# Kernel optimization log

Measured on AMD Instinct MI355X. Metric: run time of the kernel, lower is better.

Reference implementation:

```python
import jax, jax.numpy as jnp
import numpy as np

N = 100000   # n_nodes
E = 600000   # n_edges
D = 128      # cfg_node_encoding_dim
L = 4        # nr_layers
EPS = 1e-5


def setup_inputs() -> dict:
    key = jax.random.key(0)
    k0, k1, k2, k3 = jax.random.split(key, 4)
    x = jax.random.normal(k0, (N, D), dtype=jnp.float32)
    edge_index = jax.random.randint(k1, (2, E), 0, N, dtype=jnp.int32)
    W = jax.random.normal(k2, (L, D, D), dtype=jnp.float32) * (1.0 / np.sqrt(D))
    b = jax.random.normal(k3, (L, D), dtype=jnp.float32) * 0.01
    gamma = jnp.ones((L, D), dtype=jnp.float32)
    beta = jnp.zeros((L, D), dtype=jnp.float32)
    return {"x": x, "W": W, "b": b, "gamma": gamma, "beta": beta,
            "edge_index": edge_index}


def _gcn_layer(x, W, b, src_sl, dst_sl, norm):
    # PyG GCNConv: h = x @ W, then symmetric-normalized aggregation + bias
    h = x @ W                                  # [N, D]
    msg = h[src_sl] * norm[:, None]            # [E+N, D] gather + scale
    out = jax.ops.segment_sum(msg, dst_sl, num_segments=N)  # scatter-add
    return out + b


def _layer_norm(x, gamma, beta):
    mu = jnp.mean(x, axis=-1, keepdims=True)
    var = jnp.mean(jnp.square(x - mu), axis=-1, keepdims=True)
    return (x - mu) * jax.lax.rsqrt(var + EPS) * gamma + beta


def reference(x, W, b, gamma, beta, edge_index):
    src, dst = edge_index[0], edge_index[1]
    loops = jnp.arange(N, dtype=edge_index.dtype)
    src_sl = jnp.concatenate([src, loops])     # add_self_loops=True
    dst_sl = jnp.concatenate([dst, loops])
    deg = jax.ops.segment_sum(jnp.ones(E + N, dtype=x.dtype), dst_sl,
                              num_segments=N)
    dinv = jnp.where(deg > 0, jax.lax.rsqrt(deg), 0.0)
    norm = dinv[src_sl] * dinv[dst_sl]         # D^{-1/2} (A+I) D^{-1/2}
    h = x
    for i in range(L):
        h = _gcn_layer(h, W[i], b[i], src_sl, dst_sl, norm)
        h = jax.nn.relu(h)
        # dropout is identity in eval mode
        h = _layer_norm(h, gamma[i], beta[i])
    return h
```

## Files before the change

kernel.cpp:

```cpp
#include <hip/hip_runtime.h>
#include <hip/hip_bf16.h>

#define D_DIM 128
#define AST 136
#define CST 132

typedef __attribute__((ext_vector_type(8))) short short8v;
typedef __attribute__((ext_vector_type(4))) short short4v;
typedef __attribute__((ext_vector_type(4))) float floatx4;

__device__ __forceinline__ short f2bf(float x) {
    unsigned u = __builtin_bit_cast(unsigned, x);
    unsigned r = u + 0x7fff + ((u >> 16) & 1);
    return (short)(r >> 16);
}
__device__ __forceinline__ float bflo(unsigned p) {
    return __builtin_bit_cast(float, p << 16);
}
__device__ __forceinline__ float bfhi(unsigned p) {
    return __builtin_bit_cast(float, p & 0xffff0000u);
}


__global__ __launch_bounds__(256) void init_kernel(int* __restrict__ deg,
                                                   int* __restrict__ packedi,
                                                   int* __restrict__ ovcnt, int n16) {
    int i = blockIdx.x * blockDim.x + threadIdx.x;
    if (i < n16) {
        packedi[i] = i >> 4;
        if ((i & 15) == 0) deg[i >> 4] = 0;
    }
    if (i == 0) *ovcnt = 0;
}

__global__ void fill2_kernel(const int* __restrict__ src, const int* __restrict__ dst,
                             int* __restrict__ deg, int* __restrict__ packedi,
                             int2* __restrict__ ov, int* __restrict__ ovcnt, int e) {
    int i = blockIdx.x * blockDim.x + threadIdx.x;
    if (i >= e) return;
    int s = src[i], d = dst[i];
    int j = atomicAdd(&deg[d], 1);
    if (j < 16) {
        packedi[(size_t)d * 16 + j] = s;
    } else {
        int k = atomicAdd(ovcnt, 1);
        ov[k] = make_int2(d, s);
    }
}

__global__ void dinv_kernel(const int* __restrict__ deg, float* __restrict__ dinv, int n) {
    int i = blockIdx.x * blockDim.x + threadIdx.x;
    if (i < n) dinv[i] = rsqrtf((float)deg[i] + 1.0f);
}

__global__ __launch_bounds__(256) void wt_prep_kernel(const float* __restrict__ W,
                                                      short* __restrict__ Wt, int total) {
    int o = blockIdx.x * blockDim.x + threadIdx.x;
    if (o >= total) return;
    int l = o >> 14;
    int r = o & 16383;
    int nn = r >> 7;
    int k  = r & 127;
    Wt[o] = f2bf(W[(size_t)l * 16384 + (size_t)k * 128 + nn]);
}

template <bool IN_F32>
__global__ __launch_bounds__(256) void gemm_mfma_kernel(const void* __restrict__ Xv,
                                                        const short* __restrict__ Wt,
                                                        short* __restrict__ H, int n) {
    __shared__ short Alds[64 * AST];
    const int t    = threadIdx.x;
    const int wv   = t >> 6;
    const int lane = t & 63;
    const int m    = lane & 15;
    const int quad = lane >> 4;
    const int row0 = blockIdx.x * 64;

    short8v bfr[2][4];
    #pragma unroll
    for (int c = 0; c < 2; ++c) {
        const short* bp = Wt + (size_t)((wv * 2 + c) * 16 + m) * D_DIM + quad * 8;
        #pragma unroll
        for (int kt = 0; kt < 4; ++kt)
            bfr[c][kt] = *(const short8v*)(bp + kt * 32);
    }

    if constexpr (IN_F32) {
        const float* X = (const float*)Xv;
        #pragma unroll
        for (int i = 0; i < 8; ++i) {
            int q  = t + i * 256;
            int r  = q >> 5;
            int k4 = q & 31;
            int row = row0 + r;
            float4 v = make_float4(0.f, 0.f, 0.f, 0.f);
            if (row < n) v = *(const float4*)(X + (size_t)row * D_DIM + k4 * 4);
            short4v s;
            s.x = f2bf(v.x); s.y = f2bf(v.y); s.z = f2bf(v.z); s.w = f2bf(v.w);
            *(short4v*)(&Alds[r * AST + k4 * 4]) = s;
        }
    } else {
        const short* X = (const short*)Xv;
        #pragma unroll
        for (int i = 0; i < 4; ++i) {
            int q  = t + i * 256;
            int r  = q >> 4;
            int kc = q & 15;
            int row = row0 + r;
            short8v v = {0,0,0,0,0,0,0,0};
            if (row < n) v = *(const short8v*)(X + (size_t)row * D_DIM + kc * 8);
            *(short8v*)(&Alds[r * AST + kc * 8]) = v;
        }
    }
    __syncthreads();

    floatx4 acc[4][2];
    #pragma unroll
    for (int rt = 0; rt < 4; ++rt) {
        const short* ab = &Alds[(rt * 16 + m) * AST + quad * 8];
        short8v afr[4];
        #pragma unroll
        for (int kt = 0; kt < 4; ++kt) afr[kt] = *(const short8v*)(ab + kt * 32);

        #pragma unroll
        for (int c = 0; c < 2; ++c) {
            floatx4 a = (floatx4){0.f, 0.f, 0.f, 0.f};
            #pragma unroll
            for (int kt = 0; kt < 4; ++kt)
                a = __builtin_amdgcn_mfma_f32_16x16x32_bf16(afr[kt], bfr[c][kt], a, 0, 0, 0);
            acc[rt][c] = a;
        }
    }
    __syncthreads();

    #pragma unroll
    for (int rt = 0; rt < 4; ++rt) {
        #pragma unroll
        for (int c = 0; c < 2; ++c) {
            const int col = (wv * 2 + c) * 16 + m;
            #pragma unroll
            for (int r = 0; r < 4; ++r)
                Alds[(rt * 16 + quad * 4 + r) * CST + col] = f2bf(acc[rt][c][r]);
        }
    }
    __syncthreads();

    #pragma unroll
    for (int i = 0; i < 4; ++i) {
        int q  = t + i * 256;
        int r  = q >> 4;
        int kc = q & 15;
        int row = row0 + r;
        if (row < n)
            *(short8v*)(H + (size_t)row * D_DIM + kc * 8) = *(const short8v*)(&Alds[r * CST + kc * 8]);
    }
}

template <bool OUT_BF16>
__global__ __launch_bounds__(256) void agg_kernel(const short* __restrict__ Hb,
                                                  const int* __restrict__ packedi,
                                                  const int* __restrict__ deg,
                                                  const float* __restrict__ dinv,
                                                  const int2* __restrict__ ov,
                                                  const int* __restrict__ ovcnt,
                                                  const float* __restrict__ bias,
                                                  const float* __restrict__ gamma,
                                                  const float* __restrict__ beta,
                                                  void* __restrict__ Yv, int n) {
    const int wave = __builtin_amdgcn_readfirstlane(threadIdx.x >> 6);
    const int lane = threadIdx.x & 63;
    const int vA = (blockIdx.x * 4 + wave) * 2;
    if (vA >= n) return;
    const bool hasB = (vA + 1) < n;
    const int vB = hasB ? vA + 1 : vA;

    const int cntA = deg[vA];
    const int cntB = hasB ? deg[vB] : 0;
    const float dvA = dinv[vA];
    const float dvB = dinv[vB];

    const int sl = lane & 31;
    const int pk = packedi[(size_t)vA * 16 + (hasB ? sl : (sl & 15))];
    const float2 bb = ((const float2*)bias)[lane];
    const float2 gg = ((const float2*)gamma)[lane];
    const float2 be = ((const float2*)beta)[lane];
    const unsigned psA = ((const unsigned*)(Hb + (size_t)vA * D_DIM))[lane];
    const unsigned psB = ((const unsigned*)(Hb + (size_t)vB * D_DIM))[lane];

    float axA = bflo(psA) * dvA;
    float ayA = bfhi(psA) * dvA;
    float axB = bflo(psB) * dvB;
    float ayB = bfhi(psB) * dvB;

    unsigned p[16];
    float    w[16];
    #pragma unroll
    for (int j = 0; j < 8; ++j) {
        const int sA = __builtin_amdgcn_readlane(pk, j);
        const int sB = __builtin_amdgcn_readlane(pk, 16 + j);
        p[j]     = ((const unsigned*)(Hb + (size_t)sA * D_DIM))[lane];
        p[8 + j] = ((const unsigned*)(Hb + (size_t)sB * D_DIM))[lane];
        w[j]     = (j < cntA) ? dinv[sA] : 0.f;
        w[8 + j] = (j < cntB) ? dinv[sB] : 0.f;
    }
    #pragma unroll
    for (int j = 0; j < 8; ++j) {
        axA = fmaf(w[j], bflo(p[j]), axA);
        ayA = fmaf(w[j], bfhi(p[j]), ayA);
        axB = fmaf(w[8 + j], bflo(p[8 + j]), axB);
        ayB = fmaf(w[8 + j], bfhi(p[8 + j]), ayB);
    }
    if ((cntA > 8) | (cntB > 8)) {
        #pragma unroll
        for (int j = 0; j < 4; ++j) {
            const int sA = __builtin_amdgcn_readlane(pk, 8 + j);
            const int sB = __builtin_amdgcn_readlane(pk, 24 + j);
            p[j]     = ((const unsigned*)(Hb + (size_t)sA * D_DIM))[lane];
            p[4 + j] = ((const unsigned*)(Hb + (size_t)sB * D_DIM))[lane];
            w[j]     = (8 + j < cntA) ? dinv[sA] : 0.f;
            w[4 + j] = (8 + j < cntB) ? dinv[sB] : 0.f;
        }
        #pragma unroll
        for (int j = 0; j < 4; ++j) {
            axA = fmaf(w[j], bflo(p[j]), axA);
            ayA = fmaf(w[j], bfhi(p[j]), ayA);
            axB = fmaf(w[4 + j], bflo(p[4 + j]), axB);
            ayB = fmaf(w[4 + j], bfhi(p[4 + j]), ayB);
        }
        if ((cntA > 12) | (cntB > 12)) {
            #pragma unroll
            for (int j = 0; j < 4; ++j) {
                const int sA = __builtin_amdgcn_readlane(pk, 12 + j);
                const int sB = __builtin_amdgcn_readlane(pk, 28 + j);
                p[j]     = ((const unsigned*)(Hb + (size_t)sA * D_DIM))[lane];
                p[4 + j] = ((const unsigned*)(Hb + (size_t)sB * D_DIM))[lane];
                w[j]     = (12 + j < cntA) ? dinv[sA] : 0.f;
                w[4 + j] = (12 + j < cntB) ? dinv[sB] : 0.f;
            }
            #pragma unroll
            for (int j = 0; j < 4; ++j) {
                axA = fmaf(w[j], bflo(p[j]), axA);
                ayA = fmaf(w[j], bfhi(p[j]), ayA);
                axB = fmaf(w[4 + j], bflo(p[4 + j]), axB);
                ayB = fmaf(w[4 + j], bfhi(p[4 + j]), ayB);
            }
        }
        if ((cntA > 16) | (cntB > 16)) {
            const int oc = *ovcnt;
            for (int k = 0; k < oc; ++k) {
                const int2 eo = ov[k];
                if ((eo.x == vA) | (eo.x == vB)) {
                    const float ws = dinv[eo.y];
                    const unsigned q = ((const unsigned*)(Hb + (size_t)eo.y * D_DIM))[lane];
                    if (eo.x == vA) {
                        axA = fmaf(ws, bflo(q), axA);
                        ayA = fmaf(ws, bfhi(q), ayA);
                    } else {
                        axB = fmaf(ws, bflo(q), axB);
                        ayB = fmaf(ws, bfhi(q), ayB);
                    }
                }
            }
        }
    }

    #pragma unroll
    for (int s = 0; s < 2; ++s) {
        if (s == 1 && !hasB) break;
        const float dv = s ? dvB : dvA;
        float a0 = fmaxf(fmaf(dv, (s ? axB : axA), bb.x), 0.f);
        float a1 = fmaxf(fmaf(dv, (s ? ayB : ayA), bb.y), 0.f);
        float s1 = a0 + a1;
        float s2 = a0 * a0 + a1 * a1;
        #pragma unroll
        for (int m = 1; m < 64; m <<= 1) {
            s1 += __shfl_xor(s1, m, 64);
            s2 += __shfl_xor(s2, m, 64);
        }
        const float mu  = s1 * (1.f / 128.f);
        const float var = s2 * (1.f / 128.f) - mu * mu;
        const float rs  = rsqrtf(var + 1e-5f);
        const float o0 = (a0 - mu) * rs * gg.x + be.x;
        const float o1 = (a1 - mu) * rs * gg.y + be.y;
        const int v = s ? vB : vA;
        if constexpr (OUT_BF16) {
            unsigned pack = (unsigned)(unsigned short)f2bf(o0) |
                            ((unsigned)(unsigned short)f2bf(o1) << 16);
            ((unsigned*)((short*)Yv + (size_t)v * D_DIM))[lane] = pack;
        } else {
            float2 o; o.x = o0; o.y = o1;
            ((float2*)((float*)Yv + (size_t)v * D_DIM))[lane] = o;
        }
    }
}


extern "C" void kernel_launch(void* const* d_in, const int* in_sizes, int n_in,
                              void* d_out, int out_size, void* d_ws, size_t ws_size,
                              hipStream_t stream) {
    const float* x     = (const float*)d_in[0];
    const float* W     = (const float*)d_in[1];
    const float* bias  = (const float*)d_in[2];
    const float* gamma = (const float*)d_in[3];
    const float* beta  = (const float*)d_in[4];
    const int*   edges = (const int*)d_in[5];

    const int N = in_sizes[0] / D_DIM;
    const int E = in_sizes[5] / 2;
    const int L = in_sizes[1] / (D_DIM * D_DIM);

    const int* src = edges;
    const int* dst = edges + E;

    char* w = (char*)d_ws;
    short* Hb      = (short*)w; w += (size_t)N * D_DIM * sizeof(short);
    short* Act     = (short*)w; w += (size_t)N * D_DIM * sizeof(short);
    int*   deg     = (int*)w;   w += (size_t)((N + 3) & ~3) * sizeof(int);
    int*   packedi = (int*)w;   w += (size_t)N * 16 * sizeof(int);
    float* dinv    = (float*)w; w += (size_t)((N + 3) & ~3) * sizeof(float);
    int2*  ov      = (int2*)w;  w += (size_t)E * sizeof(int2);
    int*   ovcnt   = (int*)w;   w += 16;
    short* Wt      = (short*)w; w += (size_t)L * D_DIM * D_DIM * sizeof(short);

    init_kernel<<<(N * 16 + 255) / 256, 256, 0, stream>>>(deg, packedi, ovcnt, N * 16);
    fill2_kernel<<<(E + 255) / 256, 256, 0, stream>>>(src, dst, deg, packedi, ov, ovcnt, E);
    dinv_kernel<<<(N + 255) / 256, 256, 0, stream>>>(deg, dinv, N);

    const int WT_TOTAL = L * D_DIM * D_DIM;
    wt_prep_kernel<<<(WT_TOTAL + 255) / 256, 256, 0, stream>>>(W, Wt, WT_TOTAL);

    const int GB = (N + 63) / 64;
    const int AB = (N + 7) / 8;

    gemm_mfma_kernel<true><<<GB, 256, 0, stream>>>(x, Wt, Hb, N);
    agg_kernel<true><<<AB, 256, 0, stream>>>(Hb, packedi, deg, dinv, ov, ovcnt,
                                             bias, gamma, beta, Act, N);
    for (int l = 1; l < L - 1; ++l) {
        gemm_mfma_kernel<false><<<GB, 256, 0, stream>>>(Act, Wt + (size_t)l * D_DIM * D_DIM, Hb, N);
        agg_kernel<true><<<AB, 256, 0, stream>>>(Hb, packedi, deg, dinv, ov, ovcnt,
                                                 bias + (size_t)l * D_DIM,
                                                 gamma + (size_t)l * D_DIM,
                                                 beta + (size_t)l * D_DIM, Act, N);
    }
    {
        int l = L - 1;
        gemm_mfma_kernel<false><<<GB, 256, 0, stream>>>(Act, Wt + (size_t)l * D_DIM * D_DIM, Hb, N);
        agg_kernel<false><<<AB, 256, 0, stream>>>(Hb, packedi, deg, dinv, ov, ovcnt,
                                                  bias + (size_t)l * D_DIM,
                                                  gamma + (size_t)l * D_DIM,
                                                  beta + (size_t)l * D_DIM, d_out, N);
    }
}
```

Before: 341.3 us.

## Pack degree into adjacency record and compute dinv on the fly in aggregation

Stores each node's degree counter in slot 0 of its 16-int adjacency record, with up to 15 neighbours after it. This removes the separate deg and dinv arrays and the dinv kernel, and merges the init and weight-transpose kernels into one prep kernel. The aggregation kernel gets neighbour degrees with one gather per lane and computes rsqrt in-register, broadcasting weights via readlane instead of doing per-edge dinv loads. In exchange, one fewer inline slot pushes more nodes into the slow overflow scan, and rsqrt is recomputed in every layer.

```diff
diff --git a/kernel.cpp b/kernel.cpp
--- a/kernel.cpp
+++ b/kernel.cpp
@@ -20,48 +20,40 @@
 __device__ __forceinline__ float bfhi(unsigned p) {
     return __builtin_bit_cast(float, p & 0xffff0000u);
 }
-
-
-__global__ __launch_bounds__(256) void init_kernel(int* __restrict__ deg,
-                                                   int* __restrict__ packedi,
-                                                   int* __restrict__ ovcnt, int n16) {
+__device__ __forceinline__ float rdlanef(float v, int l) {
+    return __builtin_bit_cast(float, __builtin_amdgcn_readlane(__builtin_bit_cast(int, v), l));
+}
+
+
+__global__ __launch_bounds__(256) void prep_kernel(int4* __restrict__ rec4, int nrec4,
+                                                   const float* __restrict__ W,
+                                                   short* __restrict__ Wt, int wt_total,
+                                                   int* __restrict__ ovcnt) {
     int i = blockIdx.x * blockDim.x + threadIdx.x;
-    if (i < n16) {
-        packedi[i] = i >> 4;
-        if ((i & 15) == 0) deg[i >> 4] = 0;
+    if (i < nrec4) rec4[i] = make_int4(0, 0, 0, 0);
+    if (i < wt_total) {
+        int l = i >> 14;
+        int r = i & 16383;
+        int nn = r >> 7;
+        int k  = r & 127;
+        Wt[i] = f2bf(W[(size_t)l * 16384 + (size_t)k * 128 + nn]);
     }
     if (i == 0) *ovcnt = 0;
 }
 
 __global__ void fill2_kernel(const int* __restrict__ src, const int* __restrict__ dst,
-                             int* __restrict__ deg, int* __restrict__ packedi,
+                             int* __restrict__ rec,
                              int2* __restrict__ ov, int* __restrict__ ovcnt, int e) {
     int i = blockIdx.x * blockDim.x + threadIdx.x;
     if (i >= e) return;
     int s = src[i], d = dst[i];
-    int j = atomicAdd(&deg[d], 1);
-    if (j < 16) {
-        packedi[(size_t)d * 16 + j] = s;
+    int j = atomicAdd(&rec[(size_t)d * 16], 1);
+    if (j < 15) {
+        rec[(size_t)d * 16 + 1 + j] = s;
     } else {
         int k = atomicAdd(ovcnt, 1);
         ov[k] = make_int2(d, s);
     }
-}
-
-__global__ void dinv_kernel(const int* __restrict__ deg, float* __restrict__ dinv, int n) {
-    int i = blockIdx.x * blockDim.x + threadIdx.x;
-    if (i < n) dinv[i] = rsqrtf((float)deg[i] + 1.0f);
-}
-
-__global__ __launch_bounds__(256) void wt_prep_kernel(const float* __restrict__ W,
-                                                      short* __restrict__ Wt, int total) {
-    int o = blockIdx.x * blockDim.x + threadIdx.x;
-    if (o >= total) return;
-    int l = o >> 14;
-    int r = o & 16383;
-    int nn = r >> 7;
-    int k  = r & 127;
-    Wt[o] = f2bf(W[(size_t)l * 16384 + (size_t)k * 128 + nn]);
 }
 
 template <bool IN_F32>
@@ -158,9 +150,7 @@
 
 template <bool OUT_BF16>
 __global__ __launch_bounds__(256) void agg_kernel(const short* __restrict__ Hb,
-                                                  const int* __restrict__ packedi,
-                                                  const int* __restrict__ deg,
-                                                  const float* __restrict__ dinv,
+                                                  const int* __restrict__ rec,
                                                   const int2* __restrict__ ov,
                                                   const int* __restrict__ ovcnt,
                                                   const float* __restrict__ bias,
@@ -174,51 +164,61 @@
     const bool hasB = (vA + 1) < n;
     const int vB = hasB ? vA + 1 : vA;
 
-    const int cntA = deg[vA];
-    const int cntB = hasB ? deg[vB] : 0;
-    const float dvA = dinv[vA];
-    const float dvB = dinv[vB];
-
     const int sl = lane & 31;
-    const int pk = packedi[(size_t)vA * 16 + (hasB ? sl : (sl & 15))];
+    const int pk = rec[(size_t)vA * 16 + (hasB ? sl : (sl & 15))];
     const float2 bb = ((const float2*)bias)[lane];
     const float2 gg = ((const float2*)gamma)[lane];
     const float2 be = ((const float2*)beta)[lane];
     const unsigned psA = ((const unsigned*)(Hb + (size_t)vA * D_DIM))[lane];
     const unsigned psB = ((const unsigned*)(Hb + (size_t)vB * D_DIM))[lane];
+    const int pkc = min(max(pk, 0), n - 1);
+    const int dnb = rec[(size_t)pkc * 16];
+
+    const int cntA = __builtin_amdgcn_readlane(pk, 0);
+    const int cntB = hasB ? __builtin_amdgcn_readlane(pk, 16) : 0;
+    const float dvA = rsqrtf((float)cntA + 1.0f);
+    const float dvB = rsqrtf((float)cntB + 1.0f);
+
+    const int slotIdx = (lane & 15) - 1;
+    const int cntL = (lane & 16) ? cntB : cntA;
+    const int cap  = cntL < 15 ? cntL : 15;
+    const float wv = ((unsigned)slotIdx < (unsigned)cap && lane < 32)
+                       ? rsqrtf((float)dnb + 1.0f) : 0.f;
 
     float axA = bflo(psA) * dvA;
     float ayA = bfhi(psA) * dvA;
     float axB = bflo(psB) * dvB;
     float ayB = bfhi(psB) * dvB;
 
-    unsigned p[16];
-    float    w[16];
-    #pragma unroll
-    for (int j = 0; j < 8; ++j) {
-        const int sA = __builtin_amdgcn_readlane(pk, j);
-        const int sB = __builtin_amdgcn_readlane(pk, 16 + j);
-        p[j]     = ((const unsigned*)(Hb + (size_t)sA * D_DIM))[lane];
-        p[8 + j] = ((const unsigned*)(Hb + (size_t)sB * D_DIM))[lane];
-        w[j]     = (j < cntA) ? dinv[sA] : 0.f;
-        w[8 + j] = (j < cntB) ? dinv[sB] : 0.f;
-    }
-    #pragma unroll
-    for (int j = 0; j < 8; ++j) {
-        axA = fmaf(w[j], bflo(p[j]), axA);
-        ayA = fmaf(w[j], bfhi(p[j]), ayA);
-        axB = fmaf(w[8 + j], bflo(p[8 + j]), axB);
-        ayB = fmaf(w[8 + j], bfhi(p[8 + j]), ayB);
-    }
-    if ((cntA > 8) | (cntB > 8)) {
+    {
+        unsigned p[14]; float w[14];
+        #pragma unroll
+        for (int j = 0; j < 7; ++j) {
+            const int sA = __builtin_amdgcn_readlane(pk, 1 + j);
+            const int sB = __builtin_amdgcn_readlane(pk, 17 + j);
+            p[j]     = ((const unsigned*)(Hb + (size_t)sA * D_DIM))[lane];
+            p[7 + j] = ((const unsigned*)(Hb + (size_t)sB * D_DIM))[lane];
+            w[j]     = rdlanef(wv, 1 + j);
+            w[7 + j] = rdlanef(wv, 17 + j);
+        }
+        #pragma unroll
+        for (int j = 0; j < 7; ++j) {
+            axA = fmaf(w[j], bflo(p[j]), axA);
+            ayA = fmaf(w[j], bfhi(p[j]), ayA);
+            axB = fmaf(w[7 + j], bflo(p[7 + j]), axB);
+            ayB = fmaf(w[7 + j], bfhi(p[7 + j]), ayB);
+        }
+    }
+    if ((cntA > 7) | (cntB > 7)) {
+        unsigned p[8]; float w[8];
         #pragma unroll
         for (int j = 0; j < 4; ++j) {
             const int sA = __builtin_amdgcn_readlane(pk, 8 + j);
             const int sB = __builtin_amdgcn_readlane(pk, 24 + j);
             p[j]     = ((const unsigned*)(Hb + (size_t)sA * D_DIM))[lane];
             p[4 + j] = ((const unsigned*)(Hb + (size_t)sB * D_DIM))[lane];
-            w[j]     = (8 + j < cntA) ? dinv[sA] : 0.f;
-            w[4 + j] = (8 + j < cntB) ? dinv[sB] : 0.f;
+            w[j]     = rdlanef(wv, 8 + j);
+            w[4 + j] = rdlanef(wv, 24 + j);
         }
         #pragma unroll
         for (int j = 0; j < 4; ++j) {
@@ -227,15 +227,15 @@
             axB = fmaf(w[4 + j], bflo(p[4 + j]), axB);
             ayB = fmaf(w[4 + j], bfhi(p[4 + j]), ayB);
         }
-        if ((cntA > 12) | (cntB > 12)) {
+        if ((cntA > 11) | (cntB > 11)) {
             #pragma unroll
             for (int j = 0; j < 4; ++j) {
                 const int sA = __builtin_amdgcn_readlane(pk, 12 + j);
                 const int sB = __builtin_amdgcn_readlane(pk, 28 + j);
                 p[j]     = ((const unsigned*)(Hb + (size_t)sA * D_DIM))[lane];
                 p[4 + j] = ((const unsigned*)(Hb + (size_t)sB * D_DIM))[lane];
-                w[j]     = (12 + j < cntA) ? dinv[sA] : 0.f;
-                w[4 + j] = (12 + j < cntB) ? dinv[sB] : 0.f;
+                w[j]     = rdlanef(wv, 12 + j);
+                w[4 + j] = rdlanef(wv, 28 + j);
             }
             #pragma unroll
             for (int j = 0; j < 4; ++j) {
@@ -244,20 +244,21 @@
                 axB = fmaf(w[4 + j], bflo(p[4 + j]), axB);
                 ayB = fmaf(w[4 + j], bfhi(p[4 + j]), ayB);
             }
-        }
-        if ((cntA > 16) | (cntB > 16)) {
-            const int oc = *ovcnt;
-            for (int k = 0; k < oc; ++k) {
-                const int2 eo = ov[k];
-                if ((eo.x == vA) | (eo.x == vB)) {
-                    const float ws = dinv[eo.y];
-                    const unsigned q = ((const unsigned*)(Hb + (size_t)eo.y * D_DIM))[lane];
-                    if (eo.x == vA) {
-                        axA = fmaf(ws, bflo(q), axA);
-                        ayA = fmaf(ws, bfhi(q), ayA);
-                    } else {
-                        axB = fmaf(ws, bflo(q), axB);
-                        ayB = fmaf(ws, bfhi(q), ayB);
+            if ((cntA > 15) | (cntB > 15)) {
+                const int oc = *ovcnt;
+                for (int k = 0; k < oc; ++k) {
+                    const int2 eo = ov[k];
+                    if ((eo.x == vA) | (eo.x == vB)) {
+                        const int sdeg = rec[(size_t)eo.y * 16];
+                        const float ws = rsqrtf((float)sdeg + 1.0f);
+                        const unsigned q = ((const unsigned*)(Hb + (size_t)eo.y * D_DIM))[lane];
+                        if (eo.x == vA) {
+                            axA = fmaf(ws, bflo(q), axA);
+                            ayA = fmaf(ws, bfhi(q), ayA);
+                        } else {
+                            axB = fmaf(ws, bflo(q), axB);
+                            ayB = fmaf(ws, bfhi(q), ayB);
+                        }
                     }
                 }
             }
@@ -313,31 +314,29 @@
     const int* dst = edges + E;
 
     char* w = (char*)d_ws;
-    short* Hb      = (short*)w; w += (size_t)N * D_DIM * sizeof(short);
-    short* Act     = (short*)w; w += (size_t)N * D_DIM * sizeof(short);
-    int*   deg     = (int*)w;   w += (size_t)((N + 3) & ~3) * sizeof(int);
-    int*   packedi = (int*)w;   w += (size_t)N * 16 * sizeof(int);
-    float* dinv    = (float*)w; w += (size_t)((N + 3) & ~3) * sizeof(float);
-    int2*  ov      = (int2*)w;  w += (size_t)E * sizeof(int2);
-    int*   ovcnt   = (int*)w;   w += 16;
-    short* Wt      = (short*)w; w += (size_t)L * D_DIM * D_DIM * sizeof(short);
-
-    init_kernel<<<(N * 16 + 255) / 256, 256, 0, stream>>>(deg, packedi, ovcnt, N * 16);
-    fill2_kernel<<<(E + 255) / 256, 256, 0, stream>>>(src, dst, deg, packedi, ov, ovcnt, E);
-    dinv_kernel<<<(N + 255) / 256, 256, 0, stream>>>(deg, dinv, N);
+    short* Hb    = (short*)w; w += (size_t)N * D_DIM * sizeof(short);
+    short* Act   = (short*)w; w += (size_t)N * D_DIM * sizeof(short);
+    int*   rec   = (int*)w;   w += (size_t)N * 16 * sizeof(int);
+    int2*  ov    = (int2*)w;  w += (size_t)E * sizeof(int2);
+    int*   ovcnt = (int*)w;   w += 16;
+    short* Wt    = (short*)w; w += (size_t)L * D_DIM * D_DIM * sizeof(short);
 
     const int WT_TOTAL = L * D_DIM * D_DIM;
-    wt_prep_kernel<<<(WT_TOTAL + 255) / 256, 256, 0, stream>>>(W, Wt, WT_TOTAL);
+    const int NREC4 = N * 4;
+    const int PREP_T = NREC4 > WT_TOTAL ? NREC4 : WT_TOTAL;
+    prep_kernel<<<(PREP_T + 255) / 256, 256, 0, stream>>>((int4*)rec, NREC4, W, Wt,
+                                                          WT_TOTAL, ovcnt);
+    fill2_kernel<<<(E + 255) / 256, 256, 0, stream>>>(src, dst, rec, ov, ovcnt, E);
 
     const int GB = (N + 63) / 64;
     const int AB = (N + 7) / 8;
 
     gemm_mfma_kernel<true><<<GB, 256, 0, stream>>>(x, Wt, Hb, N);
-    agg_kernel<true><<<AB, 256, 0, stream>>>(Hb, packedi, deg, dinv, ov, ovcnt,
+    agg_kernel<true><<<AB, 256, 0, stream>>>(Hb, rec, ov, ovcnt,
                                              bias, gamma, beta, Act, N);
     for (int l = 1; l < L - 1; ++l) {
         gemm_mfma_kernel<false><<<GB, 256, 0, stream>>>(Act, Wt + (size_t)l * D_DIM * D_DIM, Hb, N);
-        agg_kernel<true><<<AB, 256, 0, stream>>>(Hb, packedi, deg, dinv, ov, ovcnt,
+        agg_kernel<true><<<AB, 256, 0, stream>>>(Hb, rec, ov, ovcnt,
                                                  bias + (size_t)l * D_DIM,
                                                  gamma + (size_t)l * D_DIM,
                                                  beta + (size_t)l * D_DIM, Act, N);
@@ -345,7 +344,7 @@
     {
         int l = L - 1;
         gemm_mfma_kernel<false><<<GB, 256, 0, stream>>>(Act, Wt + (size_t)l * D_DIM * D_DIM, Hb, N);
-        agg_kernel<false><<<AB, 256, 0, stream>>>(Hb, packedi, deg, dinv, ov, ovcnt,
+        agg_kernel<false><<<AB, 256, 0, stream>>>(Hb, rec, ov, ovcnt,
                                                   bias + (size_t)l * D_DIM,
                                                   gamma + (size_t)l * D_DIM,
                                                   beta + (size_t)l * D_DIM, d_out, N);
```

Measured after the change: 364.8 us. +6.9%, slower.
